# Performance work log

Hardware: AMD Instinct MI355X
Metric: run time of the kernel (lower is better)

## Reference

```python
import jax, jax.numpy as jnp
import numpy as np

N_EMBD = 384
N_HEAD = 6
HEAD_SIZE = N_EMBD // N_HEAD  # 64
BLOCK = 64
EPS = 1e-5


def _layernorm(x, g, b):
    mu = jnp.mean(x, axis=-1, keepdims=True)
    var = jnp.mean(jnp.square(x - mu), axis=-1, keepdims=True)
    return (x - mu) * jax.lax.rsqrt(var + EPS) * g + b


def setup_inputs() -> dict:
    key = jax.random.key(0)
    ks = jax.random.split(key, 12)
    s = 0.02
    return {
        "x": jax.random.normal(ks[0], (1024, BLOCK, N_EMBD), dtype=jnp.float32),
        "ln1_g": jnp.ones((N_EMBD,), jnp.float32),
        "ln1_b": jnp.zeros((N_EMBD,), jnp.float32),
        "Wq": jax.random.normal(ks[1], (N_HEAD, N_EMBD, HEAD_SIZE), jnp.float32) * s,
        "Wk": jax.random.normal(ks[2], (N_HEAD, N_EMBD, HEAD_SIZE), jnp.float32) * s,
        "Wv": jax.random.normal(ks[3], (N_HEAD, N_EMBD, HEAD_SIZE), jnp.float32) * s,
        "Wo": jax.random.normal(ks[4], (N_EMBD, N_EMBD), jnp.float32) * s,
        "bo": jnp.zeros((N_EMBD,), jnp.float32),
        "ln2_g": jnp.ones((N_EMBD,), jnp.float32),
        "ln2_b": jnp.zeros((N_EMBD,), jnp.float32),
        "W1": jax.random.normal(ks[5], (N_EMBD, 4 * N_EMBD), jnp.float32) * s,
        "b1": jnp.zeros((4 * N_EMBD,), jnp.float32),
        "W2": jax.random.normal(ks[6], (4 * N_EMBD, N_EMBD), jnp.float32) * s,
        "b2": jnp.zeros((N_EMBD,), jnp.float32),
    }


def reference(x, ln1_g, ln1_b, Wq, Wk, Wv, Wo, bo, ln2_g, ln2_b, W1, b1, W2, b2):
    B, T, C = x.shape
    # --- multi-head causal self-attention on ln1(x) ---
    xn = _layernorm(x, ln1_g, ln1_b)
    q = jnp.einsum('btc,hcd->bhtd', xn, Wq)
    k = jnp.einsum('btc,hcd->bhtd', xn, Wk)
    v = jnp.einsum('btc,hcd->bhtd', xn, Wv)
    scale = HEAD_SIZE ** -0.5
    att = jnp.einsum('bhtd,bhsd->bhts', q, k) * scale
    causal = jnp.tril(jnp.ones((T, T), bool))
    att = jnp.where(causal, att, -jnp.inf)
    att = jax.nn.softmax(att, axis=-1)  # dropout is identity at eval
    out = jnp.einsum('bhts,bhsd->bhtd', att, v)
    out = out.transpose(0, 2, 1, 3).reshape(B, T, C)  # concat heads
    x = x + out @ Wo + bo
    # --- feed-forward on ln2(x) ---
    xn2 = _layernorm(x, ln2_g, ln2_b)
    h = jax.nn.relu(xn2 @ W1 + b1)
    x = x + h @ W2 + b2
    return x
```

## Files before the change

kernel.cpp:

```cpp
#include <hip/hip_runtime.h>

#define TT 64
#define CC 384
#define NH 6
#define HID 1536
#define LDX 392
#define LDH 72

typedef __bf16 bf16x8 __attribute__((ext_vector_type(8)));
typedef float f32x4 __attribute__((ext_vector_type(4)));
typedef unsigned short us8 __attribute__((ext_vector_type(8)));

#define MFMA(a, b, c) __builtin_amdgcn_mfma_f32_16x16x32_bf16(a, b, c, 0, 0, 0)
#define WAITVM(N) asm volatile("s_waitcnt vmcnt(" #N ")" ::: "memory")

static __device__ __forceinline__ unsigned short f2bf(float f) {
  unsigned u = __builtin_bit_cast(unsigned, f);
  u += 0x7FFFu + ((u >> 16) & 1u);
  return (unsigned short)(u >> 16);
}
static __device__ __forceinline__ float bf2f(unsigned short h) {
  unsigned u = ((unsigned)h) << 16;
  return __builtin_bit_cast(float, u);
}
static __device__ __forceinline__ bf16x8 ld8(const unsigned short* p) {
  return __builtin_bit_cast(bf16x8, *reinterpret_cast<const us8*>(p));
}
static __device__ __forceinline__ void glds16(const unsigned short* g, unsigned short* l) {
  __builtin_amdgcn_global_load_lds(
      (const __attribute__((address_space(1))) void*)g,
      (__attribute__((address_space(3))) void*)l, 16, 0, 0);
}

__global__ void prep_w(const float* __restrict__ Wq, const float* __restrict__ Wk,
                       const float* __restrict__ Wv, const float* __restrict__ Wo,
                       const float* __restrict__ W1, const float* __restrict__ W2,
                       unsigned short* __restrict__ ws) {
  const int T0 = 1152 * 384;
  const int T1 = T0 + 384 * 384;
  const int T2 = T1 + 1536 * 384;
  const int T3 = T2 + 384 * 1536;
  for (int i = blockIdx.x * blockDim.x + threadIdx.x; i < T3; i += gridDim.x * blockDim.x) {
    float v;
    if (i < T0) {
      int n = i / 384, k = i % 384;
      int hh = n / 192, j = n % 192;
      const float* W = (j < 64) ? Wq : (j < 128) ? Wk : Wv;
      int d = (j < 64) ? j : (j < 128) ? j - 64 : j - 128;
      v = W[((size_t)hh * 384 + k) * 64 + d];
    } else if (i < T1) {
      int i2 = i - T0; int n = i2 / 384, k = i2 % 384;
      v = Wo[(size_t)k * 384 + n];
    } else if (i < T2) {
      int i2 = i - T1; int n = i2 / 384, k = i2 % 384;
      v = W1[(size_t)k * 1536 + n];
    } else {
      int i2 = i - T2; int n = i2 / 1536, k = i2 % 1536;
      v = W2[(size_t)k * 384 + n];
    }
    ws[i] = f2bf(v);
  }
}

__global__ __launch_bounds__(256, 2)
void attn_fwd(const float* __restrict__ x,
              const float* __restrict__ ln1g, const float* __restrict__ ln1b,
              const float* __restrict__ bo,
              const unsigned short* __restrict__ Wqkv,
              const unsigned short* __restrict__ WoT,
              float* __restrict__ x2) {
  __shared__ unsigned short sXN[TT * LDX];
  __shared__ unsigned short sHEAD[3 * TT * LDH];
  unsigned short* sQ = sHEAD;
  unsigned short* sK = sHEAD + TT * LDH;
  unsigned short* sV = sHEAD + 2 * TT * LDH;

  const int b = blockIdx.x;
  const int tid = threadIdx.x;
  const int wv = tid >> 6;
  const int ln = tid & 63;
  const int l16 = ln & 15;
  const int lg = ln >> 4;
  const float* xb = x + (size_t)b * TT * CC;
  const f32x4 Z4 = {0.f, 0.f, 0.f, 0.f};

#pragma unroll 1
  for (int r = wv * 16; r < wv * 16 + 16; ++r) {
    float v[6], s = 0.f, sq = 0.f;
#pragma unroll
    for (int j = 0; j < 6; ++j) { v[j] = xb[r * CC + ln + 64 * j]; s += v[j]; sq += v[j] * v[j]; }
#pragma unroll
    for (int off = 32; off; off >>= 1) { s += __shfl_xor(s, off); sq += __shfl_xor(sq, off); }
    float mu = s * (1.f / CC);
    float rs = rsqrtf(sq * (1.f / CC) - mu * mu + 1e-5f);
#pragma unroll
    for (int j = 0; j < 6; ++j) {
      int c = ln + 64 * j;
      sXN[r * LDX + c] = f2bf((v[j] - mu) * rs * ln1g[c] + ln1b[c]);
    }
  }
  __syncthreads();

  f32x4 pacc[4][6];
#pragma unroll
  for (int m = 0; m < 4; ++m)
#pragma unroll
    for (int c = 0; c < 6; ++c) pacc[m][c] = Z4;

  const unsigned short* prow[6];
#pragma unroll
  for (int c = 0; c < 6; ++c)
    prow[c] = WoT + (size_t)(wv * 96 + c * 16 + l16) * CC + 8 * lg;

#pragma unroll 1
  for (int h = 0; h < NH; ++h) {
    const unsigned short* wrow[3];
#pragma unroll
    for (int c = 0; c < 3; ++c)
      wrow[c] = Wqkv + (size_t)(h * 192 + wv * 48 + c * 16 + l16) * CC + 8 * lg;

    f32x4 qacc[4][3];
#pragma unroll
    for (int m = 0; m < 4; ++m)
#pragma unroll
      for (int c = 0; c < 3; ++c) qacc[m][c] = Z4;

    bf16x8 bpre[2][3];
#pragma unroll
    for (int c = 0; c < 3; ++c) bpre[0][c] = ld8(wrow[c] + 0);
#pragma unroll
    for (int c = 0; c < 3; ++c) bpre[1][c] = ld8(wrow[c] + 32);
#pragma unroll
    for (int kk = 0; kk < CC; kk += 32) {
      const int slot = (kk >> 5) & 1;
      bf16x8 bcur[3];
#pragma unroll
      for (int c = 0; c < 3; ++c) bcur[c] = bpre[slot][c];
      if (kk + 64 < CC) {
#pragma unroll
        for (int c = 0; c < 3; ++c) bpre[slot][c] = ld8(wrow[c] + kk + 64);
      }
      bf16x8 a[4];
#pragma unroll
      for (int m = 0; m < 4; ++m)
        a[m] = ld8(&sXN[(m * 16 + l16) * LDX + kk + 8 * lg]);
      __builtin_amdgcn_s_setprio(1);
#pragma unroll
      for (int c = 0; c < 3; ++c)
#pragma unroll
        for (int m = 0; m < 4; ++m) qacc[m][c] = MFMA(a[m], bcur[c], qacc[m][c]);
      __builtin_amdgcn_s_setprio(0);
    }
    __syncthreads();
#pragma unroll
    for (int m = 0; m < 4; ++m)
#pragma unroll
      for (int c = 0; c < 3; ++c) {
        int n = wv * 48 + c * 16 + l16;
#pragma unroll
        for (int rg = 0; rg < 4; ++rg) {
          int t = m * 16 + lg * 4 + rg;
          unsigned short bv = f2bf(qacc[m][c][rg]);
          if (n < 64) sQ[t * LDH + n] = bv;
          else if (n < 128) sK[t * LDH + (n - 64)] = bv;
          else sV[(n - 128) * LDH + t] = bv;
        }
      }
    __syncthreads();

    f32x4 sacc[4];
#pragma unroll
    for (int c = 0; c < 4; ++c) sacc[c] = Z4;
#pragma unroll
    for (int kk = 0; kk < 64; kk += 32) {
      bf16x8 a = ld8(&sQ[(wv * 16 + l16) * LDH + kk + 8 * lg]);
#pragma unroll
      for (int c = 0; c < 4; ++c) {
        bf16x8 bb = ld8(&sK[(c * 16 + l16) * LDH + kk + 8 * lg]);
        sacc[c] = MFMA(a, bb, sacc[c]);
      }
    }
#pragma unroll
    for (int rg = 0; rg < 4; ++rg) {
      int row = wv * 16 + lg * 4 + rg;
      float e[4], mx = -1e30f;
#pragma unroll
      for (int c = 0; c < 4; ++c) {
        int col = c * 16 + l16;
        float vv = sacc[c][rg] * 0.125f;
        e[c] = (col <= row) ? vv : -1e30f;
        mx = fmaxf(mx, e[c]);
      }
#pragma unroll
      for (int off = 8; off; off >>= 1) mx = fmaxf(mx, __shfl_xor(mx, off));
      float sum = 0.f;
#pragma unroll
      for (int c = 0; c < 4; ++c) {
        int col = c * 16 + l16;
        e[c] = (col <= row) ? __expf(e[c] - mx) : 0.f;
        sum += e[c];
      }
#pragma unroll
      for (int off = 8; off; off >>= 1) sum += __shfl_xor(sum, off);
      float inv = 1.f / sum;
#pragma unroll
      for (int c = 0; c < 4; ++c)
        sQ[row * LDH + c * 16 + l16] = f2bf(e[c] * inv);
    }

    bf16x8 pb[2][6];
#pragma unroll
    for (int s2 = 0; s2 < 2; ++s2)
#pragma unroll
      for (int c = 0; c < 6; ++c)
        pb[s2][c] = ld8(prow[c] + h * 64 + 32 * s2);

    f32x4 oacc[4];
#pragma unroll
    for (int c = 0; c < 4; ++c) oacc[c] = Z4;
#pragma unroll
    for (int kk = 0; kk < 64; kk += 32) {
      bf16x8 a = ld8(&sQ[(wv * 16 + l16) * LDH + kk + 8 * lg]);
#pragma unroll
      for (int c = 0; c < 4; ++c) {
        bf16x8 bb = ld8(&sV[(c * 16 + l16) * LDH + kk + 8 * lg]);
        oacc[c] = MFMA(a, bb, oacc[c]);
      }
    }
    __syncthreads();
#pragma unroll
    for (int c = 0; c < 4; ++c)
#pragma unroll
      for (int rg = 0; rg < 4; ++rg) {
        int t = wv * 16 + lg * 4 + rg;
        sK[t * LDH + c * 16 + l16] = f2bf(oacc[c][rg]);
      }
    __syncthreads();

    __builtin_amdgcn_s_setprio(1);
#pragma unroll
    for (int kk = 0; kk < 64; kk += 32) {
      const int slot = kk >> 5;
      bf16x8 a[4];
#pragma unroll
      for (int m = 0; m < 4; ++m)
        a[m] = ld8(&sK[(m * 16 + l16) * LDH + kk + 8 * lg]);
#pragma unroll
      for (int c = 0; c < 6; ++c)
#pragma unroll
        for (int m = 0; m < 4; ++m) pacc[m][c] = MFMA(a[m], pb[slot][c], pacc[m][c]);
    }
    __builtin_amdgcn_s_setprio(0);
  }

  float* xo = x2 + (size_t)b * TT * CC;
#pragma unroll
  for (int m = 0; m < 4; ++m)
#pragma unroll
    for (int c = 0; c < 6; ++c) {
      int n = wv * 96 + c * 16 + l16;
      float bov = bo[n];
#pragma unroll
      for (int rg = 0; rg < 4; ++rg) {
        int t = m * 16 + lg * 4 + rg;
        xo[t * CC + n] = xb[t * CC + n] + pacc[m][c][rg] + bov;
      }
    }
}

__global__ __launch_bounds__(512, 2)
void mlp_fwd(const float* __restrict__ ln2g, const float* __restrict__ ln2b,
             const float* __restrict__ b1, const float* __restrict__ b2,
             const unsigned short* __restrict__ W1T,
             const unsigned short* __restrict__ W2T,
             float* xo) {
  __shared__ unsigned short sXN[128 * 384];
  __shared__ unsigned short sH[128 * 64];
  __shared__ unsigned short sW[8 * 3072];

  const int bp = blockIdx.x;
  const int tid = threadIdx.x;
  const int wv = tid >> 6;
  const int ln = tid & 63;
  const int l16 = ln & 15;
  const int lg = ln >> 4;
  const int g = wv >> 2;
  const int p = wv & 3;
  float* xb = xo + (size_t)bp * 128 * CC;
  const f32x4 Z4 = {0.f, 0.f, 0.f, 0.f};
  unsigned short* myW = sW + wv * 3072;

#pragma unroll 1
  for (int r = wv * 16; r < wv * 16 + 16; ++r) {
    float v[6], s = 0.f, sq = 0.f;
#pragma unroll
    for (int j = 0; j < 6; ++j) { v[j] = xb[r * CC + ln + 64 * j]; s += v[j]; sq += v[j] * v[j]; }
#pragma unroll
    for (int off = 32; off; off >>= 1) { s += __shfl_xor(s, off); sq += __shfl_xor(sq, off); }
    float mu = s * (1.f / CC);
    float rs = rsqrtf(sq * (1.f / CC) - mu * mu + 1e-5f);
#pragma unroll
    for (int j = 0; j < 6; ++j) {
      int c = ln + 64 * j;
      sXN[r * 384 + (c ^ ((r & 7) << 3))] = f2bf((v[j] - mu) * rs * ln2g[c] + ln2b[c]);
    }
  }
  __syncthreads();

  const int w1r = ln >> 3;
  const int w1k = ((ln & 7) ^ (ln >> 3)) << 3;
  const int w2r = ln >> 2;
  const int w2k = (((ln & 3) ^ ((ln >> 3) & 3))) << 3;
  const int rsw = (l16 & 7) << 3;

  f32x4 macc[8][3];
#pragma unroll
  for (int m = 0; m < 8; ++m)
#pragma unroll
    for (int c = 0; c < 3; ++c) macc[m][c] = Z4;

#pragma unroll 1
  for (int ch = 0; ch < 24; ++ch) {
    f32x4 hacc[4];
#pragma unroll
    for (int m = 0; m < 4; ++m) hacc[m] = Z4;

    const unsigned short* w1g = W1T + (size_t)(ch * 64 + p * 16 + w1r) * CC + w1k;
#pragma unroll
    for (int j = 0; j < 2; ++j) glds16(w1g + (size_t)(j * 8) * CC, myW + j * 512);
    int cb = 0;
#pragma unroll 1
    for (int s = 0; s < 6; ++s) {
      if (s < 5) {
        const unsigned short* gsrc = w1g + (s + 1) * 64;
        unsigned short* d = myW + (cb ^ 1) * 1024;
#pragma unroll
        for (int j = 0; j < 2; ++j) glds16(gsrc + (size_t)(j * 8) * CC, d + j * 512);
        WAITVM(2);
      } else {
        WAITVM(0);
      }
#pragma unroll
      for (int kk2 = 0; kk2 < 2; ++kk2) {
        bf16x8 a[4];
#pragma unroll
        for (int m = 0; m < 4; ++m)
          a[m] = ld8(&sXN[(g * 64 + m * 16 + l16) * 384 + ((s * 64 + kk2 * 32 + 8 * lg) ^ rsw)]);
        bf16x8 bb = ld8(&myW[cb * 1024 + l16 * 64 + ((kk2 * 32 + 8 * lg) ^ rsw)]);
        __builtin_amdgcn_s_setprio(1);
#pragma unroll
        for (int m = 0; m < 4; ++m) hacc[m] = MFMA(a[m], bb, hacc[m]);
        __builtin_amdgcn_s_setprio(0);
      }
      cb ^= 1;
    }
    __syncthreads();

    const unsigned short* w2g = W2T + (size_t)(wv * 48 + w2r) * HID + ch * 64 + w2k;
#pragma unroll
    for (int j = 0; j < 3; ++j) glds16(w2g + (size_t)(j * 16) * HID, myW + j * 512);

    {
      float b1v = b1[ch * 64 + p * 16 + l16];
#pragma unroll
      for (int m = 0; m < 4; ++m)
#pragma unroll
        for (int rg = 0; rg < 4; ++rg) {
          int row = g * 64 + m * 16 + lg * 4 + rg;
          int col = p * 16 + l16;
          sH[row * 64 + (col ^ ((row & 7) << 3))] = f2bf(fmaxf(hacc[m][rg] + b1v, 0.f));
        }
    }
    __syncthreads();

    cb = 0;
#pragma unroll 1
    for (int s = 0; s < 2; ++s) {
      if (s == 0) {
#pragma unroll
        for (int j = 0; j < 3; ++j) glds16(w2g + 32 + (size_t)(j * 16) * HID, myW + 1536 + j * 512);
      } else {
        WAITVM(0);
      }
      bf16x8 a[8];
#pragma unroll
      for (int m = 0; m < 8; ++m)
        a[m] = ld8(&sH[(m * 16 + l16) * 64 + ((s * 32 + 8 * lg) ^ rsw)]);
      __builtin_amdgcn_s_setprio(1);
#pragma unroll
      for (int c = 0; c < 3; ++c) {
        int rloc = c * 16 + l16;
        bf16x8 bb = ld8(&myW[cb * 1536 + rloc * 32 + ((8 * lg) ^ (((rloc >> 1) & 3) << 3))]);
#pragma unroll
        for (int m = 0; m < 8; ++m) macc[m][c] = MFMA(a[m], bb, macc[m][c]);
      }
      __builtin_amdgcn_s_setprio(0);
      cb ^= 1;
    }
  }

#pragma unroll
  for (int m = 0; m < 8; ++m)
#pragma unroll
    for (int c = 0; c < 3; ++c) {
      int n = wv * 48 + c * 16 + l16;
      float b2v = b2[n];
#pragma unroll
      for (int rg = 0; rg < 4; ++rg) {
        int t = m * 16 + lg * 4 + rg;
        size_t idx = (size_t)t * CC + n;
        float x2v = xb[idx];
        xb[idx] = x2v + macc[m][c][rg] + b2v;
      }
    }
}

extern "C" void kernel_launch(void* const* d_in, const int* in_sizes, int n_in,
                              void* d_out, int out_size, void* d_ws, size_t ws_size,
                              hipStream_t stream) {
  const float* x    = (const float*)d_in[0];
  const float* ln1g = (const float*)d_in[1];
  const float* ln1b = (const float*)d_in[2];
  const float* Wq   = (const float*)d_in[3];
  const float* Wk   = (const float*)d_in[4];
  const float* Wv   = (const float*)d_in[5];
  const float* Wo   = (const float*)d_in[6];
  const float* bo   = (const float*)d_in[7];
  const float* ln2g = (const float*)d_in[8];
  const float* ln2b = (const float*)d_in[9];
  const float* W1   = (const float*)d_in[10];
  const float* b1   = (const float*)d_in[11];
  const float* W2   = (const float*)d_in[12];
  const float* b2   = (const float*)d_in[13];
  unsigned short* ws = (unsigned short*)d_ws;

  const size_t need = (size_t)(1152 * 384 + 384 * 384 + 1536 * 384 + 384 * 1536) * 2;
  if (ws_size < need) return;

  hipLaunchKernelGGL(prep_w, dim3(1024), dim3(256), 0, stream, Wq, Wk, Wv, Wo, W1, W2, ws);

  const unsigned short* Wqkv = ws;
  const unsigned short* WoT  = ws + 1152 * 384;
  const unsigned short* W1T  = WoT + 384 * 384;
  const unsigned short* W2T  = W1T + 1536 * 384;
  int nblk = in_sizes[0] / (TT * CC);

  hipLaunchKernelGGL(attn_fwd, dim3(nblk), dim3(256), 0, stream,
                     x, ln1g, ln1b, bo, Wqkv, WoT, (float*)d_out);
  hipLaunchKernelGGL(mlp_fwd, dim3(nblk / 2), dim3(512), 0, stream,
                     ln2g, ln2b, b1, b2, W1T, W2T, (float*)d_out);
}
```

Measured before the change: 471.1 us.

## Restructure MLP kernel to one sequence per block with cross-chunk weight prefetch

The MLP kernel now processes 64 tokens per block instead of 128, with each of 8 waves owning 16 hidden columns of a 128-wide hidden chunk. Both GEMMs are fully unrolled and software-pipelined: W1 uses a triple-buffered prefetch, and the next chunk's W1 loads are issued during the current chunk's W2 compute, removing the stalls at chunk boundaries. Halving the rows per block doubles the grid and cuts the accumulator registers, but each block now reads the full weight set for only 64 rows, which doubles total weight traffic from L2. The larger per-wave shared buffer also raises LDS use, which may limit blocks per CU.

```diff
diff --git a/kernel.cpp b/kernel.cpp
--- a/kernel.cpp
+++ b/kernel.cpp
@@ -274,133 +274,139 @@
              const unsigned short* __restrict__ W1T,
              const unsigned short* __restrict__ W2T,
              float* xo) {
-  __shared__ unsigned short sXN[128 * 384];
-  __shared__ unsigned short sH[128 * 64];
-  __shared__ unsigned short sW[8 * 3072];
-
-  const int bp = blockIdx.x;
+  __shared__ unsigned short sXN[TT * 384];
+  __shared__ unsigned short sH[TT * 128];
+  __shared__ unsigned short sW[8 * 6144];
+
+  const int b = blockIdx.x;
   const int tid = threadIdx.x;
   const int wv = tid >> 6;
   const int ln = tid & 63;
   const int l16 = ln & 15;
   const int lg = ln >> 4;
-  const int g = wv >> 2;
-  const int p = wv & 3;
-  float* xb = xo + (size_t)bp * 128 * CC;
+  float* xb = xo + (size_t)b * TT * CC;
   const f32x4 Z4 = {0.f, 0.f, 0.f, 0.f};
-  unsigned short* myW = sW + wv * 3072;
-
-#pragma unroll 1
-  for (int r = wv * 16; r < wv * 16 + 16; ++r) {
-    float v[6], s = 0.f, sq = 0.f;
-#pragma unroll
-    for (int j = 0; j < 6; ++j) { v[j] = xb[r * CC + ln + 64 * j]; s += v[j]; sq += v[j] * v[j]; }
-#pragma unroll
-    for (int off = 32; off; off >>= 1) { s += __shfl_xor(s, off); sq += __shfl_xor(sq, off); }
-    float mu = s * (1.f / CC);
-    float rs = rsqrtf(sq * (1.f / CC) - mu * mu + 1e-5f);
-#pragma unroll
-    for (int j = 0; j < 6; ++j) {
-      int c = ln + 64 * j;
-      sXN[r * 384 + (c ^ ((r & 7) << 3))] = f2bf((v[j] - mu) * rs * ln2g[c] + ln2b[c]);
-    }
-  }
-  __syncthreads();
-
+  unsigned short* myW = sW + wv * 6144;
+
+  const int rsw = (l16 & 7) << 3;
   const int w1r = ln >> 3;
   const int w1k = ((ln & 7) ^ (ln >> 3)) << 3;
   const int w2r = ln >> 2;
   const int w2k = (((ln & 3) ^ ((ln >> 3) & 3))) << 3;
-  const int rsw = (l16 & 7) << 3;
-
-  f32x4 macc[8][3];
-#pragma unroll
-  for (int m = 0; m < 8; ++m)
+
+#pragma unroll 1
+  for (int r = wv * 8; r < wv * 8 + 8; ++r) {
+    float v[6], s = 0.f, sq = 0.f;
+#pragma unroll
+    for (int j = 0; j < 6; ++j) { v[j] = xb[r * CC + ln + 64 * j]; s += v[j]; sq += v[j] * v[j]; }
+#pragma unroll
+    for (int off = 32; off; off >>= 1) { s += __shfl_xor(s, off); sq += __shfl_xor(sq, off); }
+    float mu = s * (1.f / CC);
+    float rs = rsqrtf(sq * (1.f / CC) - mu * mu + 1e-5f);
+#pragma unroll
+    for (int j = 0; j < 6; ++j) {
+      int c = ln + 64 * j;
+      sXN[r * 384 + (c ^ ((r & 7) << 3))] = f2bf((v[j] - mu) * rs * ln2g[c] + ln2b[c]);
+    }
+  }
+  __syncthreads();
+
+#define G1_STAGE(P, SS) do {                                                 \
+    glds16((P) + (SS) * 64, myW + ((SS) % 3) * 1024);                        \
+    glds16((P) + (SS) * 64 + (size_t)8 * CC, myW + ((SS) % 3) * 1024 + 512); \
+  } while (0)
+
+#define G1_COMP(SS) do {                                                              \
+    _Pragma("unroll")                                                                 \
+    for (int kk2 = 0; kk2 < 2; ++kk2) {                                               \
+      bf16x8 a_[4];                                                                   \
+      _Pragma("unroll")                                                               \
+      for (int m = 0; m < 4; ++m)                                                     \
+        a_[m] = ld8(&sXN[(m * 16 + l16) * 384 +                                       \
+                         (((SS) * 64 + kk2 * 32 + 8 * lg) ^ rsw)]);                   \
+      bf16x8 bb_ = ld8(&myW[((SS) % 3) * 1024 + l16 * 64 + ((kk2 * 32 + 8 * lg) ^ rsw)]); \
+      __builtin_amdgcn_s_setprio(1);                                                  \
+      _Pragma("unroll")                                                               \
+      for (int m = 0; m < 4; ++m) hacc[m] = MFMA(a_[m], bb_, hacc[m]);                \
+      __builtin_amdgcn_s_setprio(0);                                                  \
+    }                                                                                 \
+  } while (0)
+
+#define G2_STAGE(SS) do {                                                      \
+    glds16(w2g + (SS) * 32, myW + (SS) * 1536);                                \
+    glds16(w2g + (SS) * 32 + (size_t)16 * HID, myW + (SS) * 1536 + 512);       \
+    glds16(w2g + (SS) * 32 + (size_t)32 * HID, myW + (SS) * 1536 + 1024);      \
+  } while (0)
+
+#define G2_COMP(SS) do {                                                          \
+    bf16x8 a_[4];                                                                 \
+    _Pragma("unroll")                                                             \
+    for (int m = 0; m < 4; ++m)                                                   \
+      a_[m] = ld8(&sH[(m * 16 + l16) * 128 + (((SS) * 32 + 8 * lg) ^ rsw)]);      \
+    __builtin_amdgcn_s_setprio(1);                                                \
+    _Pragma("unroll")                                                             \
+    for (int c = 0; c < 3; ++c) {                                                 \
+      int rloc_ = c * 16 + l16;                                                   \
+      bf16x8 bb_ = ld8(&myW[(SS) * 1536 + rloc_ * 32 +                            \
+                            ((8 * lg) ^ (((rloc_ >> 1) & 3) << 3))]);             \
+      _Pragma("unroll")                                                           \
+      for (int m = 0; m < 4; ++m) macc[m][c] = MFMA(a_[m], bb_, macc[m][c]);      \
+    }                                                                             \
+    __builtin_amdgcn_s_setprio(0);                                                \
+  } while (0)
+
+  f32x4 macc[4][3];
+#pragma unroll
+  for (int m = 0; m < 4; ++m)
 #pragma unroll
     for (int c = 0; c < 3; ++c) macc[m][c] = Z4;
 
+  const unsigned short* w1g = W1T + (size_t)(0 * 128 + wv * 16 + w1r) * CC + w1k;
+  G1_STAGE(w1g, 0); G1_STAGE(w1g, 1); G1_STAGE(w1g, 2);
+
 #pragma unroll 1
-  for (int ch = 0; ch < 24; ++ch) {
+  for (int ch = 0; ch < 12; ++ch) {
     f32x4 hacc[4];
 #pragma unroll
     for (int m = 0; m < 4; ++m) hacc[m] = Z4;
 
-    const unsigned short* w1g = W1T + (size_t)(ch * 64 + p * 16 + w1r) * CC + w1k;
-#pragma unroll
-    for (int j = 0; j < 2; ++j) glds16(w1g + (size_t)(j * 8) * CC, myW + j * 512);
-    int cb = 0;
-#pragma unroll 1
-    for (int s = 0; s < 6; ++s) {
-      if (s < 5) {
-        const unsigned short* gsrc = w1g + (s + 1) * 64;
-        unsigned short* d = myW + (cb ^ 1) * 1024;
-#pragma unroll
-        for (int j = 0; j < 2; ++j) glds16(gsrc + (size_t)(j * 8) * CC, d + j * 512);
-        WAITVM(2);
-      } else {
-        WAITVM(0);
-      }
-#pragma unroll
-      for (int kk2 = 0; kk2 < 2; ++kk2) {
-        bf16x8 a[4];
-#pragma unroll
-        for (int m = 0; m < 4; ++m)
-          a[m] = ld8(&sXN[(g * 64 + m * 16 + l16) * 384 + ((s * 64 + kk2 * 32 + 8 * lg) ^ rsw)]);
-        bf16x8 bb = ld8(&myW[cb * 1024 + l16 * 64 + ((kk2 * 32 + 8 * lg) ^ rsw)]);
-        __builtin_amdgcn_s_setprio(1);
-#pragma unroll
-        for (int m = 0; m < 4; ++m) hacc[m] = MFMA(a[m], bb, hacc[m]);
-        __builtin_amdgcn_s_setprio(0);
-      }
-      cb ^= 1;
-    }
-    __syncthreads();
-
-    const unsigned short* w2g = W2T + (size_t)(wv * 48 + w2r) * HID + ch * 64 + w2k;
-#pragma unroll
-    for (int j = 0; j < 3; ++j) glds16(w2g + (size_t)(j * 16) * HID, myW + j * 512);
+    WAITVM(4); G1_COMP(0); G1_STAGE(w1g, 3);
+    WAITVM(4); G1_COMP(1); G1_STAGE(w1g, 4);
+    WAITVM(4); G1_COMP(2); G1_STAGE(w1g, 5);
+    WAITVM(4); G1_COMP(3);
+    WAITVM(2); G1_COMP(4);
+    WAITVM(0); G1_COMP(5);
+
+    const unsigned short* w2g = W2T + (size_t)(wv * 48 + w2r) * HID + ch * 128 + w2k;
+    G2_STAGE(0); G2_STAGE(1);
+    float b1v = b1[ch * 128 + wv * 16 + l16];
+    __syncthreads();
 
     {
-      float b1v = b1[ch * 64 + p * 16 + l16];
+      int nl = wv * 16 + l16;
 #pragma unroll
       for (int m = 0; m < 4; ++m)
 #pragma unroll
         for (int rg = 0; rg < 4; ++rg) {
-          int row = g * 64 + m * 16 + lg * 4 + rg;
-          int col = p * 16 + l16;
-          sH[row * 64 + (col ^ ((row & 7) << 3))] = f2bf(fmaxf(hacc[m][rg] + b1v, 0.f));
+          int t = m * 16 + lg * 4 + rg;
+          sH[t * 128 + (nl ^ ((t & 7) << 3))] = f2bf(fmaxf(hacc[m][rg] + b1v, 0.f));
         }
     }
     __syncthreads();
 
-    cb = 0;
-#pragma unroll 1
-    for (int s = 0; s < 2; ++s) {
-      if (s == 0) {
-#pragma unroll
-        for (int j = 0; j < 3; ++j) glds16(w2g + 32 + (size_t)(j * 16) * HID, myW + 1536 + j * 512);
-      } else {
-        WAITVM(0);
-      }
-      bf16x8 a[8];
-#pragma unroll
-      for (int m = 0; m < 8; ++m)
-        a[m] = ld8(&sH[(m * 16 + l16) * 64 + ((s * 32 + 8 * lg) ^ rsw)]);
-      __builtin_amdgcn_s_setprio(1);
-#pragma unroll
-      for (int c = 0; c < 3; ++c) {
-        int rloc = c * 16 + l16;
-        bf16x8 bb = ld8(&myW[cb * 1536 + rloc * 32 + ((8 * lg) ^ (((rloc >> 1) & 3) << 3))]);
-#pragma unroll
-        for (int m = 0; m < 8; ++m) macc[m][c] = MFMA(a[m], bb, macc[m][c]);
-      }
-      __builtin_amdgcn_s_setprio(0);
-      cb ^= 1;
-    }
+    int chn = (ch + 1 < 12) ? ch + 1 : 0;
+    const unsigned short* w1gn = W1T + (size_t)(chn * 128 + wv * 16 + w1r) * CC + w1k;
+
+     G2_COMP(0); G2_STAGE(2);
+    WAITVM(3);     G2_COMP(1); G2_STAGE(3);
+    WAITVM(3);     G2_COMP(2); G1_STAGE(w1gn, 0); G1_STAGE(w1gn, 1);
+    WAITVM(4);     G2_COMP(3); G1_STAGE(w1gn, 2);
+
+    w1g = w1gn;
   }
 
 #pragma unroll
-  for (int m = 0; m < 8; ++m)
+  for (int m = 0; m < 4; ++m)
 #pragma unroll
     for (int c = 0; c < 3; ++c) {
       int n = wv * 48 + c * 16 + l16;
@@ -413,6 +419,10 @@
         xb[idx] = x2v + macc[m][c][rg] + b2v;
       }
     }
+#undef G1_STAGE
+#undef G1_COMP
+#undef G2_STAGE
+#undef G2_COMP
 }
 
 extern "C" void kernel_launch(void* const* d_in, const int* in_sizes, int n_in,
@@ -447,6 +457,6 @@
 
   hipLaunchKernelGGL(attn_fwd, dim3(nblk), dim3(256), 0, stream,
                      x, ln1g, ln1b, bo, Wqkv, WoT, (float*)d_out);
-  hipLaunchKernelGGL(mlp_fwd, dim3(nblk / 2), dim3(512), 0, stream,
+  hipLaunchKernelGGL(mlp_fwd, dim3(nblk), dim3(512), 0, stream,
                      ln2g, ln2b, b1, b2, W1T, W2T, (float*)d_out);
 }
```

Measured after the change: 462.4 us. Within noise of the previous version (-1.8%).
